# Optimization experiments

Measured on AMD Instinct MI355X. Metric: run time of the kernel, lower is better.

The kernel has to match this reference:

```python
import jax, jax.numpy as jnp
import numpy as np

B, N, DI, DS, DP, DM, S = 64, 4096, 64, 64, 64, 128, 7
NUM_ITER = 3
EPS_ATTN = 1e-8
LN_EPS = 1e-5


def setup_inputs() -> dict:
    key = jax.random.key(0)
    ks = jax.random.split(key, 12)
    rn = lambda k, shp, sc=1.0: (jax.random.normal(k, shp, jnp.float32) * sc)
    return {
        "x": rn(ks[0], (B, N, DI)),
        "ln_inp_g": jnp.ones((DI,), jnp.float32),
        "ln_inp_b": jnp.zeros((DI,), jnp.float32),
        "ln_slot_g": jnp.ones((DS,), jnp.float32),
        "ln_slot_b": jnp.zeros((DS,), jnp.float32),
        "slots_init": rn(ks[1], (1, S, DS)),
        "Wk": rn(ks[2], (DI, DP), 1.0 / np.sqrt(DI)),
        "Wv": rn(ks[3], (DI, DP), 1.0 / np.sqrt(DI)),
        "Wq": rn(ks[4], (DS, DP), 1.0 / np.sqrt(DS)),
        "gru_wih": rn(ks[5], (3 * DS, DP), 1.0 / np.sqrt(DS)),
        "gru_whh": rn(ks[6], (3 * DS, DS), 1.0 / np.sqrt(DS)),
        "gru_bih": jnp.zeros((3 * DS,), jnp.float32),
        "gru_bhh": jnp.zeros((3 * DS,), jnp.float32),
        "mlp_w1": rn(ks[7], (DS, DM), 1.0 / np.sqrt(DS)),
        "mlp_b1": jnp.zeros((DM,), jnp.float32),
        "mlp_w2": rn(ks[8], (DM, DS), 1.0 / np.sqrt(DM)),
        "mlp_b2": jnp.zeros((DS,), jnp.float32),
    }


def _layernorm(x, g, b):
    m = jnp.mean(x, axis=-1, keepdims=True)
    v = jnp.mean(jnp.square(x - m), axis=-1, keepdims=True)
    return (x - m) * jax.lax.rsqrt(v + LN_EPS) * g + b


def _gru_cell(u, h, wih, whh, bih, bhh):
    # PyTorch GRUCell semantics
    gi = u @ wih.T + bih  # [*, 3*DS]
    gh = h @ whh.T + bhh
    ir, iz, inn = jnp.split(gi, 3, axis=-1)
    hr, hz, hn = jnp.split(gh, 3, axis=-1)
    r = jax.nn.sigmoid(ir + hr)
    z = jax.nn.sigmoid(iz + hz)
    n = jnp.tanh(inn + r * hn)
    return (1.0 - z) * n + z * h


def reference(x, ln_inp_g, ln_inp_b, ln_slot_g, ln_slot_b, slots_init,
              Wk, Wv, Wq, gru_wih, gru_whh, gru_bih, gru_bhh,
              mlp_w1, mlp_b1, mlp_w2, mlp_b2):
    x = _layernorm(x, ln_inp_g, ln_inp_b)          # [B,N,DI]
    k = x @ Wk                                      # [B,N,DP] (hoisted; x fixed across iters)
    v = x @ Wv                                      # [B,N,DP]
    slots = jnp.broadcast_to(slots_init, (x.shape[0], S, DS))
    scale = 1.0 / np.sqrt(DP)
    for _ in range(NUM_ITER):
        slots_prev = slots
        sn = _layernorm(slots, ln_slot_g, ln_slot_b)
        q = sn @ Wq                                 # [B,S,DP]
        attn = jnp.einsum('bnd,bsd->bns', k, q) * scale
        attn = jax.nn.softmax(attn, axis=-1) + EPS_ATTN      # softmax over slots
        weights = attn / jnp.sum(attn, axis=1, keepdims=True)  # normalize over N
        updates = jnp.einsum('bns,bnd->bsd', weights, v)     # [B,S,DP]
        h = _gru_cell(updates.reshape(-1, DP), slots_prev.reshape(-1, DS),
                      gru_wih, gru_whh, gru_bih, gru_bhh)
        slots = h.reshape(-1, S, DS)
        slots = slots + (jax.nn.relu(slots @ mlp_w1 + mlp_b1) @ mlp_w2 + mlp_b2)
    return slots
```

## Files before the change

### kernel.cpp

```cpp
#include <hip/hip_runtime.h>
#include <stdint.h>

#define L2E 1.44269504088896f

static __device__ __forceinline__ float wsum(float v) {
    #pragma unroll
    for (int m = 1; m < 64; m <<= 1) v += __shfl_xor(v, m, 64);
    return v;
}
static __device__ __forceinline__ float sigm(float x) {
    return 1.0f / (1.0f + __builtin_amdgcn_exp2f(-x * L2E));
}
static __device__ __forceinline__ float tanh_(float x) {
    const float ax = fabsf(x);
    const float t = __builtin_amdgcn_exp2f(-2.0f * ax * L2E);
    const float r = (1.0f - t) / (1.0f + t);
    return (x < 0.f) ? -r : r;
}

__global__ __launch_bounds__(256) void init_kernel(
    const float* __restrict__ s0,
    const float* __restrict__ lsg, const float* __restrict__ lsb,
    const float* __restrict__ Wq,  const float* __restrict__ Wk,
    const float* __restrict__ lig, const float* __restrict__ lib,
    const float* __restrict__ wih, const float* __restrict__ whh,
    float* __restrict__ slots, float* __restrict__ gkq, float* __restrict__ aux,
    float* __restrict__ wihT, float* __restrict__ whhT, float* __restrict__ WkT)
{
    __shared__ float wkT[4096];
    __shared__ float scr[4][64];
    const int tid = threadIdx.x, lane = tid & 63, wv = tid >> 6;
    const int idx = blockIdx.x * 256 + tid;

    if (idx < 12288) {
        const int i = idx / 192, j = idx - i * 192;
        wihT[idx] = wih[j * 64 + i];
    } else if (idx < 24576) {
        const int o = idx - 12288;
        const int i = o / 192, j = o - i * 192;
        whhT[o] = whh[j * 64 + i];
    } else {
        const int o = idx - 24576;
        const int p = o >> 6, d = o & 63;
        WkT[o] = Wk[d * 64 + p];
    }

    const int r = blockIdx.x * 4 + wv;
    const int s = r % 7;
    #pragma unroll
    for (int i = tid; i < 4096; i += 256) {
        const int d = i >> 6, p = i & 63;
        wkT[p * 64 + d] = Wk[i];
    }
    const float h = s0[s * 64 + lane];
    slots[r * 64 + lane] = h;
    __syncthreads();

    const float mean = wsum(h) * (1.0f / 64.0f);
    const float d = h - mean;
    const float var = wsum(d * d) * (1.0f / 64.0f);
    const float rs = rsqrtf(var + 1e-5f);
    const float sn = d * rs * lsg[lane] + lsb[lane];
    scr[wv][lane] = sn;
    __syncthreads();
    float q = 0.f;
    #pragma unroll 8
    for (int i = 0; i < 64; ++i) q = fmaf(scr[wv][i], Wq[i * 64 + lane], q);
    q *= 0.125f;
    __syncthreads();
    scr[wv][lane] = q;
    __syncthreads();
    float kq = 0.f;
    #pragma unroll 8
    for (int p = 0; p < 64; ++p) kq = fmaf(wkT[p * 64 + lane], scr[wv][p], kq);
    const float bk = wsum(lib[lane] * kq);
    const float gk = lig[lane] * kq;
    const float g1 = wsum(gk);
    gkq[r * 64 + lane] = gk;
    if (lane == 0) { aux[r * 2] = g1; aux[r * 2 + 1] = bk; }
}

__global__ __launch_bounds__(256) void attn_kernel(
    const float* __restrict__ x,
    const float* __restrict__ gkq, const float* __restrict__ aux,
    float* __restrict__ Ypart)
{
    __shared__ float xsh[4][32 * 65];
    __shared__ float wsh[4][32][8];
    __shared__ float gkql[448];
    __shared__ float auxl[14];
    __shared__ float ybuf[4][456];
    const int tid = threadIdx.x, lane = tid & 63, wv = tid >> 6;
    const int b = blockIdx.x >> 4, chunk = blockIdx.x & 15;

    gkql[tid] = gkq[b * 448 + tid];
    if (tid < 192) gkql[tid + 256] = gkq[b * 448 + tid + 256];
    if (tid < 14) auxl[tid] = aux[b * 14 + tid];
    __syncthreads();

    const int q5 = lane & 31, h = lane >> 5;
    float Yr[14];
    #pragma unroll
    for (int i = 0; i < 14; ++i) Yr[i] = 0.f;
    float cacc[7] = {0.f, 0.f, 0.f, 0.f, 0.f, 0.f, 0.f};

    const float* tbase = x + (((long)b * 4096) + chunk * 256 + wv * 64) * 64;
    #pragma unroll 1
    for (int pass = 0; pass < 2; ++pass) {
        const float4* src = (const float4*)(tbase + pass * 2048);
        #pragma unroll
        for (int st = 0; st < 8; ++st) {
            const float4 d4 = src[st * 64 + lane];
            const int f = (st * 64 + lane) * 4;
            const int row = f >> 6, dim = f & 63;
            float* dst = &xsh[wv][row * 65 + dim];
            dst[0] = d4.x; dst[1] = d4.y; dst[2] = d4.z; dst[3] = d4.w;
        }

        float xf[32];
        float sum = 0.f, ss = 0.f;
        const float* xr = &xsh[wv][q5 * 65 + h * 32];
        #pragma unroll
        for (int c = 0; c < 32; ++c) {
            xf[c] = xr[c];
            sum += xf[c];
            ss = fmaf(xf[c], xf[c], ss);
        }
        float acc[7];
        #pragma unroll
        for (int s = 0; s < 7; ++s) {
            float a = 0.f;
            const float* gk = &gkql[s * 64 + h * 32];
            #pragma unroll
            for (int c = 0; c < 32; ++c) a = fmaf(xf[c], gk[c], a);
            acc[s] = a;
        }
        sum += __shfl_xor(sum, 32, 64);
        ss  += __shfl_xor(ss, 32, 64);
        #pragma unroll
        for (int s = 0; s < 7; ++s) acc[s] += __shfl_xor(acc[s], 32, 64);

        const float m   = sum * (1.0f / 64.0f);
        const float var = ss * (1.0f / 64.0f) - m * m;
        const float rs  = rsqrtf(var + 1e-5f);
        const float rsm = rs * m;
        float t[7];
        #pragma unroll
        for (int s = 0; s < 7; ++s)
            t[s] = fmaf(rs, acc[s], fmaf(-rsm, auxl[2 * s], auxl[2 * s + 1]));
        float mx = t[0];
        #pragma unroll
        for (int s = 1; s < 7; ++s) mx = fmaxf(mx, t[s]);
        float e[7], se = 0.f;
        #pragma unroll
        for (int s = 0; s < 7; ++s) {
            e[s] = __builtin_amdgcn_exp2f((t[s] - mx) * L2E);
            se += e[s];
        }
        const float inv = 1.0f / se;
        #pragma unroll
        for (int s = 0; s < 7; ++s) {
            const float w = fmaf(e[s], inv, 1e-8f);
            cacc[s] += w;
            if (h == 0) wsh[wv][q5][s] = w * rs;
        }
        if (h == 0) wsh[wv][q5][7] = 0.f;

        #pragma unroll 4
        for (int r2 = 0; r2 < 16; ++r2) {
            const int rr = r2 * 2 + h;
            const float4 p0 = *(const float4*)&wsh[wv][rr][0];
            const float4 p1 = *(const float4*)&wsh[wv][rr][4];
            const float v0 = xsh[wv][rr * 65 + q5 * 2];
            const float v1 = xsh[wv][rr * 65 + q5 * 2 + 1];
            const float ps[7] = {p0.x, p0.y, p0.z, p0.w, p1.x, p1.y, p1.z};
            #pragma unroll
            for (int s = 0; s < 7; ++s) {
                Yr[2 * s]     = fmaf(ps[s], v0, Yr[2 * s]);
                Yr[2 * s + 1] = fmaf(ps[s], v1, Yr[2 * s + 1]);
            }
        }
    }

    #pragma unroll
    for (int i = 0; i < 14; ++i) Yr[i] += __shfl_xor(Yr[i], 32, 64);
    if (h == 0) {
        #pragma unroll
        for (int s = 0; s < 7; ++s) {
            ybuf[wv][s * 64 + q5 * 2]     = Yr[2 * s];
            ybuf[wv][s * 64 + q5 * 2 + 1] = Yr[2 * s + 1];
        }
    }
    #pragma unroll
    for (int s = 0; s < 7; ++s) {
        const float Cs = wsum(cacc[s]) * 0.5f;
        if (lane == 0) ybuf[wv][448 + s] = Cs;
    }
    if (lane == 1) ybuf[wv][455] = 0.f;
    __syncthreads();
    for (int i = tid; i < 455; i += 256)
        Ypart[((long)b * 16 + chunk) * 456 + i] =
            ybuf[0][i] + ybuf[1][i] + ybuf[2][i] + ybuf[3][i];
}

__global__ __launch_bounds__(256) void update_kernel(
    const float* __restrict__ Ypart, float* __restrict__ slots,
    const float* __restrict__ Wv,
    const float* __restrict__ wihT, const float* __restrict__ whhT,
    const float* __restrict__ bih,  const float* __restrict__ bhh,
    const float* __restrict__ w1,   const float* __restrict__ b1,
    const float* __restrict__ w2,   const float* __restrict__ b2,
    const float* __restrict__ lsg,  const float* __restrict__ lsb,
    const float* __restrict__ Wq,   const float* __restrict__ WkT,
    const float* __restrict__ lig,  const float* __restrict__ lib,
    float* __restrict__ gkq, float* __restrict__ aux,
    float* __restrict__ out, int last)
{
    __shared__ float red[4][64];
    __shared__ float c16[16];
    __shared__ float ash[64];
    __shared__ float ush[64];
    __shared__ float hsh[64];
    __shared__ float gish[192], ghsh[192];
    __shared__ float hnsh[64];
    __shared__ float mbsh[128];
    __shared__ float qsh[64];
    const int tid = threadIdx.x, lane = tid & 63, wv = tid >> 6;
    const int r = blockIdx.x;
    const int b = r / 7, s = r - b * 7;
    const float* Yb = Ypart + (long)b * 16 * 456;

    float yp = 0.f;
    #pragma unroll
    for (int c = 0; c < 4; ++c)
        yp += Yb[(wv * 4 + c) * 456 + s * 64 + lane];
    red[wv][lane] = yp;
    if (tid < 16) c16[tid] = Yb[tid * 456 + 448 + s];
    if (tid >= 64 && tid < 128) hsh[tid - 64] = slots[r * 64 + (tid - 64)];
    __syncthreads();

    if (tid < 64) {
        const float Yd = red[0][lane] + red[1][lane] + red[2][lane] + red[3][lane];
        float C = 0.f;
        #pragma unroll
        for (int c = 0; c < 16; ++c) C += c16[c];
        const float Z = wsum(Yd) * (1.0f / 64.0f);
        ash[lane] = (lig[lane] * (Yd - Z) + lib[lane] * C) / C;
    }
    __syncthreads();

    float up = 0.f;
    #pragma unroll
    for (int i = 0; i < 16; ++i) {
        const int ii = wv * 16 + i;
        up = fmaf(ash[ii], Wv[ii * 64 + lane], up);
    }
    red[wv][lane] = up;
    __syncthreads();
    if (tid < 64) ush[lane] = red[0][lane] + red[1][lane] + red[2][lane] + red[3][lane];
    __syncthreads();

    if (tid < 192) {
        float a1 = bih[tid], a2 = bhh[tid];
        #pragma unroll 8
        for (int i = 0; i < 64; ++i) {
            a1 = fmaf(ush[i], wihT[i * 192 + tid], a1);
            a2 = fmaf(hsh[i], whhT[i * 192 + tid], a2);
        }
        gish[tid] = a1; ghsh[tid] = a2;
    }
    __syncthreads();
    if (tid < 64) {
        const float rr = sigm(gish[tid] + ghsh[tid]);
        const float zz = sigm(gish[64 + tid] + ghsh[64 + tid]);
        const float nn = tanh_(gish[128 + tid] + rr * ghsh[128 + tid]);
        hnsh[tid] = (1.f - zz) * nn + zz * hsh[tid];
    }
    __syncthreads();

    if (tid < 128) {
        float m = b1[tid];
        #pragma unroll 8
        for (int i = 0; i < 64; ++i) m = fmaf(hnsh[i], w1[i * 128 + tid], m);
        mbsh[tid] = fmaxf(m, 0.f);
    }
    __syncthreads();

    if (tid < 64) {
        float o = b2[tid];
        #pragma unroll 8
        for (int t = 0; t < 128; ++t) o = fmaf(mbsh[t], w2[t * 64 + tid], o);
        const float snv = hnsh[tid] + o;
        slots[r * 64 + tid] = snv;
        if (last) {
            out[r * 64 + tid] = snv;
        } else {
            const float mean = wsum(snv) * (1.0f / 64.0f);
            const float d = snv - mean;
            const float var = wsum(d * d) * (1.0f / 64.0f);
            const float rs = rsqrtf(var + 1e-5f);
            const float sn = d * rs * lsg[tid] + lsb[tid];
            ash[tid] = sn;
            float q = 0.f;
            #pragma unroll 8
            for (int i = 0; i < 64; ++i) q = fmaf(ash[i], Wq[i * 64 + tid], q);
            qsh[tid] = q * 0.125f;
            float kq = 0.f;
            #pragma unroll 8
            for (int p = 0; p < 64; ++p) kq = fmaf(WkT[p * 64 + tid], qsh[p], kq);
            const float bk = wsum(lib[tid] * kq);
            const float gk = lig[tid] * kq;
            const float g1 = wsum(gk);
            gkq[r * 64 + tid] = gk;
            if (tid == 0) { aux[r * 2] = g1; aux[r * 2 + 1] = bk; }
        }
    }
}

extern "C" void kernel_launch(void* const* d_in, const int* in_sizes, int n_in,
                              void* d_out, int out_size, void* d_ws, size_t ws_size,
                              hipStream_t stream)
{
    const float* x   = (const float*)d_in[0];
    const float* lig = (const float*)d_in[1];
    const float* lib = (const float*)d_in[2];
    const float* lsg = (const float*)d_in[3];
    const float* lsb = (const float*)d_in[4];
    const float* s0  = (const float*)d_in[5];
    const float* Wk  = (const float*)d_in[6];
    const float* Wv  = (const float*)d_in[7];
    const float* Wq  = (const float*)d_in[8];
    const float* wih = (const float*)d_in[9];
    const float* whh = (const float*)d_in[10];
    const float* bih = (const float*)d_in[11];
    const float* bhh = (const float*)d_in[12];
    const float* w1  = (const float*)d_in[13];
    const float* b1  = (const float*)d_in[14];
    const float* w2  = (const float*)d_in[15];
    const float* b2  = (const float*)d_in[16];

    float* f = (float*)d_ws;
    float* gkq   = f; f += 448 * 64;
    float* aux   = f; f += 448 * 2;
    float* slots = f; f += 448 * 64;
    float* Ypart = f; f += (long)64 * 16 * 456;
    float* wihT  = f; f += 64 * 192;
    float* whhT  = f; f += 64 * 192;
    float* WkT   = f; f += 64 * 64;

    init_kernel<<<112, 256, 0, stream>>>(s0, lsg, lsb, Wq, Wk, lig, lib,
                                         wih, whh, slots, gkq, aux,
                                         wihT, whhT, WkT);
    for (int it = 0; it < 3; ++it) {
        attn_kernel<<<1024, 256, 0, stream>>>(x, gkq, aux, Ypart);
        update_kernel<<<448, 256, 0, stream>>>(
            Ypart, slots, Wv, wihT, whhT, bih, bhh, w1, b1, w2, b2,
            lsg, lsb, Wq, WkT, lig, lib, gkq, aux,
            (float*)d_out, it == 2);
    }
}
```

Before: 235.3 us.

## Register-resident attention tile: drop shared-memory staging, use 8-lane row groups

Rewrites the attention kernel so each wave reads x straight from global memory as float4 pairs, with 8 lanes covering one 64-dim token row and 8 rows per step. The gkq and aux values now live in registers instead of LDS. The softmax-weighted value accumulation happens per lane in a 7x8 register accumulator. This removes the LDS staging stores and reloads and the per-pass barrier-free LDS traffic. In exchange it adds cross-lane shuffle reductions, both per row and a larger final reduction over 56 accumulators, and raises register pressure.

```diff
diff --git a/kernel.cpp b/kernel.cpp
--- a/kernel.cpp
+++ b/kernel.cpp
@@ -85,69 +85,68 @@
     const float* __restrict__ gkq, const float* __restrict__ aux,
     float* __restrict__ Ypart)
 {
-    __shared__ float xsh[4][32 * 65];
-    __shared__ float wsh[4][32][8];
-    __shared__ float gkql[448];
-    __shared__ float auxl[14];
     __shared__ float ybuf[4][456];
     const int tid = threadIdx.x, lane = tid & 63, wv = tid >> 6;
     const int b = blockIdx.x >> 4, chunk = blockIdx.x & 15;
-
-    gkql[tid] = gkq[b * 448 + tid];
-    if (tid < 192) gkql[tid + 256] = gkq[b * 448 + tid + 256];
-    if (tid < 14) auxl[tid] = aux[b * 14 + tid];
-    __syncthreads();
-
-    const int q5 = lane & 31, h = lane >> 5;
-    float Yr[14];
-    #pragma unroll
-    for (int i = 0; i < 14; ++i) Yr[i] = 0.f;
+    const int d3 = lane & 7, r3 = lane >> 3;
+
+    float gkr[7][8];
+    #pragma unroll
+    for (int s = 0; s < 7; ++s) {
+        const float4 g0 = *(const float4*)(gkq + b * 448 + s * 64 + d3 * 8);
+        const float4 g1 = *(const float4*)(gkq + b * 448 + s * 64 + d3 * 8 + 4);
+        gkr[s][0] = g0.x; gkr[s][1] = g0.y; gkr[s][2] = g0.z; gkr[s][3] = g0.w;
+        gkr[s][4] = g1.x; gkr[s][5] = g1.y; gkr[s][6] = g1.z; gkr[s][7] = g1.w;
+    }
+    float auxg[7], auxb[7];
+    #pragma unroll
+    for (int s = 0; s < 7; ++s) {
+        auxg[s] = aux[b * 14 + 2 * s];
+        auxb[s] = aux[b * 14 + 2 * s + 1];
+    }
+
+    const float* tb = x + (((long)b * 4096) + chunk * 256 + wv * 64) * 64;
+    float Yacc[7][8];
+    #pragma unroll
+    for (int s = 0; s < 7; ++s)
+        #pragma unroll
+        for (int k = 0; k < 8; ++k) Yacc[s][k] = 0.f;
     float cacc[7] = {0.f, 0.f, 0.f, 0.f, 0.f, 0.f, 0.f};
 
-    const float* tbase = x + (((long)b * 4096) + chunk * 256 + wv * 64) * 64;
-    #pragma unroll 1
-    for (int pass = 0; pass < 2; ++pass) {
-        const float4* src = (const float4*)(tbase + pass * 2048);
-        #pragma unroll
-        for (int st = 0; st < 8; ++st) {
-            const float4 d4 = src[st * 64 + lane];
-            const int f = (st * 64 + lane) * 4;
-            const int row = f >> 6, dim = f & 63;
-            float* dst = &xsh[wv][row * 65 + dim];
-            dst[0] = d4.x; dst[1] = d4.y; dst[2] = d4.z; dst[3] = d4.w;
-        }
-
-        float xf[32];
+    #pragma unroll 2
+    for (int j = 0; j < 8; ++j) {
+        const float* xr = tb + (j * 8 + r3) * 64 + d3 * 8;
+        const float4 x0 = ((const float4*)xr)[0];
+        const float4 x1 = ((const float4*)xr)[1];
+        const float xf[8] = {x0.x, x0.y, x0.z, x0.w, x1.x, x1.y, x1.z, x1.w};
+
         float sum = 0.f, ss = 0.f;
-        const float* xr = &xsh[wv][q5 * 65 + h * 32];
-        #pragma unroll
-        for (int c = 0; c < 32; ++c) {
-            xf[c] = xr[c];
-            sum += xf[c];
-            ss = fmaf(xf[c], xf[c], ss);
-        }
-        float acc[7];
+        #pragma unroll
+        for (int k = 0; k < 8; ++k) { sum += xf[k]; ss = fmaf(xf[k], xf[k], ss); }
+        float as[7];
         #pragma unroll
         for (int s = 0; s < 7; ++s) {
             float a = 0.f;
-            const float* gk = &gkql[s * 64 + h * 32];
             #pragma unroll
-            for (int c = 0; c < 32; ++c) a = fmaf(xf[c], gk[c], a);
-            acc[s] = a;
-        }
-        sum += __shfl_xor(sum, 32, 64);
-        ss  += __shfl_xor(ss, 32, 64);
-        #pragma unroll
-        for (int s = 0; s < 7; ++s) acc[s] += __shfl_xor(acc[s], 32, 64);
-
-        const float m   = sum * (1.0f / 64.0f);
-        const float var = ss * (1.0f / 64.0f) - m * m;
-        const float rs  = rsqrtf(var + 1e-5f);
-        const float rsm = rs * m;
+            for (int k = 0; k < 8; ++k) a = fmaf(xf[k], gkr[s][k], a);
+            as[s] = a;
+        }
+        #pragma unroll
+        for (int m = 1; m < 8; m <<= 1) {
+            sum += __shfl_xor(sum, m, 64);
+            ss  += __shfl_xor(ss, m, 64);
+            #pragma unroll
+            for (int s = 0; s < 7; ++s) as[s] += __shfl_xor(as[s], m, 64);
+        }
+
+        const float mean = sum * (1.0f / 64.0f);
+        const float var  = ss * (1.0f / 64.0f) - mean * mean;
+        const float rs   = rsqrtf(var + 1e-5f);
+        const float rsm  = rs * mean;
         float t[7];
         #pragma unroll
         for (int s = 0; s < 7; ++s)
-            t[s] = fmaf(rs, acc[s], fmaf(-rsm, auxl[2 * s], auxl[2 * s + 1]));
+            t[s] = fmaf(rs, as[s], fmaf(-rsm, auxg[s], auxb[s]));
         float mx = t[0];
         #pragma unroll
         for (int s = 1; s < 7; ++s) mx = fmaxf(mx, t[s]);
@@ -158,45 +157,44 @@
             se += e[s];
         }
         const float inv = 1.0f / se;
+        float wrs[7];
         #pragma unroll
         for (int s = 0; s < 7; ++s) {
             const float w = fmaf(e[s], inv, 1e-8f);
             cacc[s] += w;
-            if (h == 0) wsh[wv][q5][s] = w * rs;
-        }
-        if (h == 0) wsh[wv][q5][7] = 0.f;
-
-        #pragma unroll 4
-        for (int r2 = 0; r2 < 16; ++r2) {
-            const int rr = r2 * 2 + h;
-            const float4 p0 = *(const float4*)&wsh[wv][rr][0];
-            const float4 p1 = *(const float4*)&wsh[wv][rr][4];
-            const float v0 = xsh[wv][rr * 65 + q5 * 2];
-            const float v1 = xsh[wv][rr * 65 + q5 * 2 + 1];
-            const float ps[7] = {p0.x, p0.y, p0.z, p0.w, p1.x, p1.y, p1.z};
+            wrs[s] = w * rs;
+        }
+        #pragma unroll
+        for (int s = 0; s < 7; ++s)
             #pragma unroll
-            for (int s = 0; s < 7; ++s) {
-                Yr[2 * s]     = fmaf(ps[s], v0, Yr[2 * s]);
-                Yr[2 * s + 1] = fmaf(ps[s], v1, Yr[2 * s + 1]);
-            }
-        }
-    }
-
-    #pragma unroll
-    for (int i = 0; i < 14; ++i) Yr[i] += __shfl_xor(Yr[i], 32, 64);
-    if (h == 0) {
+            for (int k = 0; k < 8; ++k)
+                Yacc[s][k] = fmaf(wrs[s], xf[k], Yacc[s][k]);
+    }
+
+    #pragma unroll
+    for (int m = 8; m < 64; m <<= 1)
+        #pragma unroll
+        for (int s = 0; s < 7; ++s)
+            #pragma unroll
+            for (int k = 0; k < 8; ++k)
+                Yacc[s][k] += __shfl_xor(Yacc[s][k], m, 64);
+    #pragma unroll
+    for (int s = 0; s < 7; ++s) cacc[s] = wsum(cacc[s]) * 0.125f;
+
+    if (r3 == 0) {
         #pragma unroll
         for (int s = 0; s < 7; ++s) {
-            ybuf[wv][s * 64 + q5 * 2]     = Yr[2 * s];
-            ybuf[wv][s * 64 + q5 * 2 + 1] = Yr[2 * s + 1];
-        }
-    }
-    #pragma unroll
-    for (int s = 0; s < 7; ++s) {
-        const float Cs = wsum(cacc[s]) * 0.5f;
-        if (lane == 0) ybuf[wv][448 + s] = Cs;
-    }
-    if (lane == 1) ybuf[wv][455] = 0.f;
+            *(float4*)&ybuf[wv][s * 64 + d3 * 8] =
+                make_float4(Yacc[s][0], Yacc[s][1], Yacc[s][2], Yacc[s][3]);
+            *(float4*)&ybuf[wv][s * 64 + d3 * 8 + 4] =
+                make_float4(Yacc[s][4], Yacc[s][5], Yacc[s][6], Yacc[s][7]);
+        }
+    }
+    if (lane == 0) {
+        #pragma unroll
+        for (int s = 0; s < 7; ++s) ybuf[wv][448 + s] = cacc[s];
+        ybuf[wv][455] = 0.f;
+    }
     __syncthreads();
     for (int i = tid; i < 455; i += 256)
         Ypart[((long)b * 16 + chunk) * 456 + i] =
```

Measured after the change: 259.9 us. 1.1x slower.
